# Kernel tuning notes

Measured on AMD Instinct MI355X. Metric: run time of the kernel, lower is better.

## Reference

```python
import jax, jax.numpy as jnp
import numpy as np

G = 32        # group_num
PD = 8        # primary capsule dim
OC = 10       # output caps (classes)
OD = 16       # output dim
GS = 36       # group_size = primary spatial 6*6
N_ITERS = 3   # routing iterations


def conv2d(x, w, stride):
    return jax.lax.conv_general_dilated(
        x, w, window_strides=(stride, stride), padding='VALID',
        dimension_numbers=('NCHW', 'OIHW', 'NCHW'))


def squash(x):
    l2 = jnp.sum(x * x, axis=-1, keepdims=True)
    l = jnp.sqrt(l2)
    return x * (l2 / (1.0 + l2)) / (l + 1e-8)


def setup_inputs() -> dict:
    key = jax.random.key(0)
    ks = jax.random.split(key, 6)
    B = 256
    inp = jax.random.normal(ks[0], (B, 1, 28, 28), dtype=jnp.float32)
    W1 = jax.random.normal(ks[1], (256, 1, 9, 9), dtype=jnp.float32) * 0.05
    b1 = jnp.zeros((256,), dtype=jnp.float32)
    W2 = jax.random.normal(ks[2], (G * PD, 256, 9, 9), dtype=jnp.float32) * 0.01
    b2 = jnp.zeros((G * PD,), dtype=jnp.float32)
    Wcaps = jax.random.normal(ks[3], (G, GS, PD, OC * OD), dtype=jnp.float32) * 0.01
    b_route = jnp.zeros((G, 1, GS, OC), dtype=jnp.float32)
    return {'input': inp, 'W1': W1, 'b1': b1, 'W2': W2, 'b2': b2,
            'Wcaps': Wcaps, 'b_route': b_route}


def reference(input, W1, b1, W2, b2, Wcaps, b_route):
    B = input.shape[0]
    # conv1 + relu: (B,256,20,20)
    x = jax.nn.relu(conv2d(input, W1, 1) + b1[None, :, None, None])
    # primary caps conv: (B,256,6,6)
    y = conv2d(x, W2, 2) + b2[None, :, None, None]
    H = y.shape[2]
    # (B,G,PD,H,W) -> (B,G,H,W,PD) -> (B,G,GS,PD)
    y = y.reshape(B, G, PD, H, H).transpose(0, 1, 3, 4, 2).reshape(B, G, GS, PD)
    u = squash(y)
    # capsule predictions: (B,G,GS,OC,OD)
    up = jnp.einsum('bgsi,gsio->bgso', u, Wcaps).reshape(B, G, GS, OC, OD)
    # routing logits: (B,G,GS,OC)
    b = jnp.broadcast_to(jnp.transpose(b_route, (1, 0, 2, 3)), (B, G, GS, OC))
    v = None
    for r in range(N_ITERS):
        c = jax.nn.softmax(b, axis=3)                       # (B,G,GS,OC)
        s = jnp.einsum('bgso,bgsod->bgod', c, up)           # (B,G,OC,OD)
        v = squash(s)
        if r < N_ITERS - 1:
            b = b + jnp.einsum('bgsod,bgod->bgso', up, v)
    v = v.sum(axis=1)                                       # (B,OC,OD)
    probs = jnp.sqrt(jnp.sum(v * v, axis=2))                # (B,OC)
    return v, probs
```

## Files before the change

kernel.cpp:

```cpp
#include <hip/hip_runtime.h>
#include <math.h>


typedef float floatx4 __attribute__((ext_vector_type(4)));
typedef __bf16 bf16x8 __attribute__((ext_vector_type(8)));
typedef unsigned uintx4 __attribute__((ext_vector_type(4)));

#define XHI_OFF 0u
#define XLO_OFF 52428800u
#define WHI_OFF 104857600u
#define WLO_OFF 116391936u
#define Y2_OFF  127926272u
#define VP_OFF  137363456u
#define Y2_BYTES 9437184u

#define SL_IY   88
#define SL_IMG  1760
#define SL_PAR  7072
#define SL_TOT  14144

#define TAPSTRIDE 65536

__device__ __forceinline__ void bf16split(float v, short& hs, short& ls) {
  unsigned u = __builtin_bit_cast(unsigned, v);
  unsigned r = (u + 0x7FFFu + ((u >> 16) & 1u)) & 0xFFFF0000u;
  hs = (short)(r >> 16);
  float lo = v - __builtin_bit_cast(float, r);
  unsigned u2 = __builtin_bit_cast(unsigned, lo);
  unsigned r2 = u2 + 0x7FFFu + ((u2 >> 16) & 1u);
  ls = (short)(r2 >> 16);
}

__global__ __launch_bounds__(320) void conv1_k(
    const float* __restrict__ inp, const float* __restrict__ W1,
    const float* __restrict__ b1, short* __restrict__ xhi,
    short* __restrict__ xlo) {
  __shared__ __align__(16) float img[784];
  __shared__ float wl[81 * 34];
  const int blk = blockIdx.x;
  const int b = blk >> 3;
  const int cbase = (blk & 7) * 32;
  const int t = threadIdx.x;

  const float4* src = (const float4*)(inp + b * 784);
  for (int idx = t; idx < 196; idx += 320) ((float4*)img)[idx] = src[idx];
  for (int idx = t; idx < 2592; idx += 320) {
    int c = idx / 81, tap = idx - c * 81;
    wl[tap * 34 + c] = W1[(cbase + c) * 81 + tap];
  }
  __syncthreads();

  const int oy = t >> 4;
  const int ct = t & 15;
  const int c0 = cbase + ct * 2;
  const float bias0 = b1[c0], bias1 = b1[c0 + 1];
  float acc0[20], acc1[20];
#pragma unroll
  for (int ox = 0; ox < 20; ox++) { acc0[ox] = bias0; acc1[ox] = bias1; }

#pragma unroll 1
  for (int i = 0; i < 9; i++) {
    float wr0[9], wr1[9];
#pragma unroll
    for (int j = 0; j < 9; j++) {
      float2 wv = *(const float2*)&wl[(i * 9 + j) * 34 + ct * 2];
      wr0[j] = wv.x; wr1[j] = wv.y;
    }
    float xr[28];
    const float4* rp = (const float4*)&img[(oy + i) * 28];
#pragma unroll
    for (int k = 0; k < 7; k++) {
      float4 v = rp[k];
      xr[4 * k] = v.x; xr[4 * k + 1] = v.y; xr[4 * k + 2] = v.z; xr[4 * k + 3] = v.w;
    }
#pragma unroll
    for (int j = 0; j < 9; j++)
#pragma unroll
      for (int ox = 0; ox < 20; ox++) {
        acc0[ox] = fmaf(xr[ox + j], wr0[j], acc0[ox]);
        acc1[ox] = fmaf(xr[ox + j], wr1[j], acc1[ox]);
      }
  }
  const long pbase = (long)(b * 400 + oy * 20) * 256 + c0;
#pragma unroll
  for (int ox = 0; ox < 20; ox++) {
    float v0 = fmaxf(acc0[ox], 0.f), v1 = fmaxf(acc1[ox], 0.f);
    short h0, l0, h1, l1;
    bf16split(v0, h0, l0);
    bf16split(v1, h1, l1);
    long a = pbase + (long)ox * 256;
    *(short2*)&xhi[a] = make_short2(h0, h1);
    *(short2*)&xlo[a] = make_short2(l0, l1);
  }
}

__global__ __launch_bounds__(256) void wtrans_k(
    const float* __restrict__ W2, short* __restrict__ whi,
    short* __restrict__ wlo) {
  __shared__ short lh[81 * 258];
  __shared__ short ll[81 * 258];
  const int blk = blockIdx.x;
  const int icg = blk & 31, ocg = blk >> 5;
  const int t = threadIdx.x;

  for (int idx = t; idx < 20736; idx += 256) {
    int c = idx / 648, r = idx - c * 648;
    int ics = r / 81, tap = r - ics * 81;
    float v = W2[(long)(ocg * 32 + c) * 20736 + icg * 648 + r];
    short h, l;
    bf16split(v, h, l);
    lh[tap * 258 + c * 8 + ics] = h;
    ll[tap * 258 + c * 8 + ics] = l;
  }
  __syncthreads();
  const long obase = (long)icg * 2048 + ocg * 256 + t;
#pragma unroll 1
  for (int tap = 0; tap < 88; tap++) {
    short h = 0, l = 0;
    if (tap < 81) { h = lh[tap * 258 + t]; l = ll[tap * 258 + t]; }
    whi[obase + (long)tap * TAPSTRIDE] = h;
    wlo[obase + (long)tap * TAPSTRIDE] = l;
  }
}

__global__ __launch_bounds__(256, 2) void conv2_k(
    const short* __restrict__ xhi, const short* __restrict__ xlo,
    const short* __restrict__ whi, const short* __restrict__ wlo,
    float* __restrict__ y2) {
  __shared__ __align__(16) short slabA[SL_TOT];

  const int blk = blockIdx.x;
  const int ks = blk & 7;
  const int mb = blk >> 3;
  const int b0 = mb * 4;
  const int t = threadIdx.x;
  const int lane = t & 63;
  const int q = lane >> 4;
  const int ln16 = lane & 15;
  const int wv = t >> 6;

  int combo[9];
#pragma unroll
  for (int mt = 0; mt < 9; mt++) {
    int row = mt * 16 + ln16;
    int im = row / 36;
    int pos = row - im * 36;
    int oy = pos / 6, ox = pos - oy * 6;
    combo[mt] = im * SL_IMG + oy * (2 * SL_IY) + ox * 8;
  }

  floatx4 acc[9][4];
#pragma unroll
  for (int mt = 0; mt < 9; mt++)
#pragma unroll
    for (int nt = 0; nt < 4; nt++) acc[mt][nt] = (floatx4)0.f;

#pragma unroll 1
  for (int icg = 0; icg < 4; icg++) {
    const int icgG = ks * 4 + icg;
    const long icoff = (long)icgG * 8;
    const long wb0 = ((long)icgG * 256 + wv * 64 + ln16) * 8 + (long)q * TAPSTRIDE;

    __syncthreads();
    for (int idx = t; idx < 1600; idx += 256) {
      int im = idx / 400, p = idx - im * 400;
      int iy = p / 20, ix = p - iy * 20;
      int dst = (ix & 1) * SL_PAR + im * SL_IMG + iy * SL_IY + (ix >> 1) * 8;
      const long src = ((long)(b0 + im) * 400 + p) * 256 + icoff;
      uintx4 vh = __builtin_nontemporal_load((const uintx4*)&xhi[src]);
      *(uintx4*)&slabA[dst] = vh;
    }
    __syncthreads();

    {
      bf16x8 cbh[4];
#pragma unroll
      for (int nt = 0; nt < 4; nt++) cbh[nt] = *(const bf16x8*)&whi[wb0 + nt * 128];
#pragma unroll 1
      for (int kst = 0; kst < 21; kst++) {
        const int t0n = (kst < 20) ? (kst + 1) * 4 : 80;
        bf16x8 nbh[4], cbl[4];
#pragma unroll
        for (int nt = 0; nt < 4; nt++) {
          nbh[nt] = *(const bf16x8*)&whi[wb0 + (long)t0n * TAPSTRIDE + nt * 128];
          cbl[nt] = *(const bf16x8*)&wlo[wb0 + (long)(kst * 4) * TAPSTRIDE + nt * 128];
        }
        const int tap = kst * 4 + q;
        const int i = tap / 9, j = tap - i * 9;
        const int aoff = (j & 1) * SL_PAR + i * SL_IY + (j >> 1) * 8;
#pragma unroll
        for (int bb = 0; bb < 3; bb++) {
          bf16x8 av[3];
#pragma unroll
          for (int m3 = 0; m3 < 3; m3++)
            av[m3] = *(const bf16x8*)&slabA[aoff + combo[bb * 3 + m3]];
#pragma unroll
          for (int nt = 0; nt < 4; nt++)
#pragma unroll
            for (int m3 = 0; m3 < 3; m3++)
              acc[bb * 3 + m3][nt] = __builtin_amdgcn_mfma_f32_16x16x32_bf16(
                  av[m3], cbh[nt], acc[bb * 3 + m3][nt], 0, 0, 0);
#pragma unroll
          for (int nt = 0; nt < 4; nt++)
#pragma unroll
            for (int m3 = 0; m3 < 3; m3++)
              acc[bb * 3 + m3][nt] = __builtin_amdgcn_mfma_f32_16x16x32_bf16(
                  av[m3], cbl[nt], acc[bb * 3 + m3][nt], 0, 0, 0);
        }
#pragma unroll
        for (int nt = 0; nt < 4; nt++) cbh[nt] = nbh[nt];
      }
    }

    __syncthreads();
    for (int idx = t; idx < 1600; idx += 256) {
      int im = idx / 400, p = idx - im * 400;
      int iy = p / 20, ix = p - iy * 20;
      int dst = (ix & 1) * SL_PAR + im * SL_IMG + iy * SL_IY + (ix >> 1) * 8;
      const long src = ((long)(b0 + im) * 400 + p) * 256 + icoff;
      uintx4 vl = __builtin_nontemporal_load((const uintx4*)&xlo[src]);
      *(uintx4*)&slabA[dst] = vl;
    }
    __syncthreads();

    {
      bf16x8 cbh[4];
#pragma unroll
      for (int nt = 0; nt < 4; nt++) cbh[nt] = *(const bf16x8*)&whi[wb0 + nt * 128];
#pragma unroll 1
      for (int kst = 0; kst < 21; kst++) {
        const int t0n = (kst < 20) ? (kst + 1) * 4 : 80;
        bf16x8 nbh[4];
#pragma unroll
        for (int nt = 0; nt < 4; nt++)
          nbh[nt] = *(const bf16x8*)&whi[wb0 + (long)t0n * TAPSTRIDE + nt * 128];
        const int tap = kst * 4 + q;
        const int i = tap / 9, j = tap - i * 9;
        const int aoff = (j & 1) * SL_PAR + i * SL_IY + (j >> 1) * 8;
#pragma unroll
        for (int bb = 0; bb < 3; bb++) {
          bf16x8 av[3];
#pragma unroll
          for (int m3 = 0; m3 < 3; m3++)
            av[m3] = *(const bf16x8*)&slabA[aoff + combo[bb * 3 + m3]];
#pragma unroll
          for (int nt = 0; nt < 4; nt++)
#pragma unroll
            for (int m3 = 0; m3 < 3; m3++)
              acc[bb * 3 + m3][nt] = __builtin_amdgcn_mfma_f32_16x16x32_bf16(
                  av[m3], cbh[nt], acc[bb * 3 + m3][nt], 0, 0, 0);
        }
#pragma unroll
        for (int nt = 0; nt < 4; nt++) cbh[nt] = nbh[nt];
      }
    }
  }

#pragma unroll
  for (int mt = 0; mt < 9; mt++)
#pragma unroll
    for (int nt = 0; nt < 4; nt++) {
      int oc = wv * 64 + nt * 16 + ln16;
      int rowb = mb * 144 + mt * 16 + q * 4;
#pragma unroll
      for (int r = 0; r < 4; r++)
        atomicAdd(&y2[(long)(rowb + r) * 256 + oc], acc[mt][nt][r]);
    }
}

__global__ __launch_bounds__(256) void caps_k(
    const float* __restrict__ y2, const float* __restrict__ b2,
    const float* __restrict__ Wcaps, const float* __restrict__ b_route,
    float* __restrict__ vpart) {
  __shared__ float u[288];
  __shared__ float usc[36];
  __shared__ float up[5760];
  __shared__ float bl[360];
  __shared__ float cl[360];
  __shared__ float sv[160];
  __shared__ float vv[160];
  __shared__ float scale[10];
  const int blk = blockIdx.x;
  const int g = blk & 31, b = blk >> 5;
  const int t = threadIdx.x;

  for (int idx = t; idx < 288; idx += 256) {
    int s = idx >> 3, d = idx & 7;
    u[idx] = y2[((long)b * 36 + s) * 256 + g * 8 + d] + b2[g * 8 + d];
  }
  for (int idx = t; idx < 360; idx += 256) bl[idx] = b_route[g * 360 + idx];
  __syncthreads();
  if (t < 36) {
    float l2 = 0.f;
#pragma unroll
    for (int d = 0; d < 8; d++) { float v = u[t * 8 + d]; l2 = fmaf(v, v, l2); }
    float l = sqrtf(l2);
    usc[t] = (l2 / (1.f + l2)) / (l + 1e-8f);
  }
  __syncthreads();
  for (int idx = t; idx < 288; idx += 256) u[idx] *= usc[idx >> 3];
  __syncthreads();
  for (int idx = t; idx < 5760; idx += 256) {
    int s = idx / 160, k = idx - s * 160;
    const float* wp = Wcaps + (g * 36 + s) * 8 * 160 + k;
    float a = 0.f;
#pragma unroll
    for (int d = 0; d < 8; d++) a = fmaf(u[s * 8 + d], wp[d * 160], a);
    up[idx] = a;
  }
  __syncthreads();

  for (int r = 0; r < 3; r++) {
    if (t < 36) {
      float m = bl[t * 10];
#pragma unroll
      for (int oc = 1; oc < 10; oc++) m = fmaxf(m, bl[t * 10 + oc]);
      float e[10]; float sum = 0.f;
#pragma unroll
      for (int oc = 0; oc < 10; oc++) { e[oc] = expf(bl[t * 10 + oc] - m); sum += e[oc]; }
      float inv = 1.f / sum;
#pragma unroll
      for (int oc = 0; oc < 10; oc++) cl[t * 10 + oc] = e[oc] * inv;
    }
    __syncthreads();
    if (t < 160) {
      const int oc = t >> 4;
      float a = 0.f;
#pragma unroll 1
      for (int s = 0; s < 36; s++) a = fmaf(cl[s * 10 + oc], up[s * 160 + t], a);
      sv[t] = a;
    }
    __syncthreads();
    if (t < 10) {
      float l2 = 0.f;
#pragma unroll
      for (int od = 0; od < 16; od++) { float v = sv[t * 16 + od]; l2 = fmaf(v, v, l2); }
      scale[t] = (l2 / (1.f + l2)) / (sqrtf(l2) + 1e-8f);
    }
    __syncthreads();
    if (t < 160) vv[t] = sv[t] * scale[t >> 4];
    __syncthreads();
    if (r < 2) {
      for (int idx = t; idx < 360; idx += 256) {
        int s = idx / 10, oc = idx - s * 10;
        float a = 0.f;
#pragma unroll
        for (int od = 0; od < 16; od++)
          a = fmaf(up[s * 160 + oc * 16 + od], vv[oc * 16 + od], a);
        bl[idx] += a;
      }
      __syncthreads();
    }
  }
  if (t < 160) vpart[(b * 32 + g) * 160 + t] = vv[t];
}

__global__ __launch_bounds__(192) void final_k(
    const float* __restrict__ vpart, float* __restrict__ out) {
  __shared__ float v[160];
  const int b = blockIdx.x, t = threadIdx.x;
  if (t < 160) {
    float a = 0.f;
#pragma unroll 4
    for (int g = 0; g < 32; g++) a += vpart[(b * 32 + g) * 160 + t];
    v[t] = a;
    out[b * 160 + t] = a;
  }
  __syncthreads();
  if (t < 10) {
    float l2 = 0.f;
#pragma unroll
    for (int od = 0; od < 16; od++) { float x = v[t * 16 + od]; l2 = fmaf(x, x, l2); }
    out[40960 + b * 10 + t] = sqrtf(l2);
  }
}

extern "C" void kernel_launch(void* const* d_in, const int* in_sizes, int n_in,
                              void* d_out, int out_size, void* d_ws, size_t ws_size,
                              hipStream_t stream) {
  const float* inp     = (const float*)d_in[0];
  const float* W1      = (const float*)d_in[1];
  const float* b1      = (const float*)d_in[2];
  const float* W2      = (const float*)d_in[3];
  const float* b2      = (const float*)d_in[4];
  const float* Wcaps   = (const float*)d_in[5];
  const float* b_route = (const float*)d_in[6];
  float* out = (float*)d_out;
  char* ws = (char*)d_ws;

  short* xhi = (short*)(ws + XHI_OFF);
  short* xlo = (short*)(ws + XLO_OFF);
  short* whi = (short*)(ws + WHI_OFF);
  short* wlo = (short*)(ws + WLO_OFF);
  float* y2  = (float*)(ws + Y2_OFF);
  float* vp  = (float*)(ws + VP_OFF);

  (void)hipMemsetAsync(y2, 0, Y2_BYTES, stream);
  conv1_k <<<2048, 320, 0, stream>>>(inp, W1, b1, xhi, xlo);
  wtrans_k<<<256, 256, 0, stream>>>(W2, whi, wlo);
  conv2_k <<<512, 256, 0, stream>>>(xhi, xlo, whi, wlo, y2);
  caps_k  <<<8192, 256, 0, stream>>>(y2, b2, Wcaps, b_route, vp);
  final_k <<<256, 192, 0, stream>>>(vp, out);
}
```

Baseline: 549.5 us.

## Write conv1 output in slab layout and double-buffer conv2 staging via LDS DMA

conv1 now stores its hi/lo bf16 activations directly in the padded, parity-split slab layout that conv2 uses. The padding columns are zero-filled, and the workspace offsets are reshuffled to fit. conv2 then copies each slab straight into LDS with global_load_lds and two buffers, so the next hi/lo slab loads while the current one feeds the MFMAs. This removes the per-element index math, the register round trip and one barrier per stage. In exchange it relies on the barrier's implicit wait for the async LDS loads to finish, and the workspace layout gets a little larger.

```diff
diff --git a/kernel.cpp b/kernel.cpp
--- a/kernel.cpp
+++ b/kernel.cpp
@@ -7,17 +7,17 @@
 typedef unsigned uintx4 __attribute__((ext_vector_type(4)));
 
 #define XHI_OFF 0u
-#define XLO_OFF 52428800u
-#define WHI_OFF 104857600u
-#define WLO_OFF 116391936u
-#define Y2_OFF  127926272u
-#define VP_OFF  137363456u
+#define XLO_OFF 58720256u
+#define WHI_OFF 117440512u
+#define WLO_OFF 128974848u
+#define Y2_OFF  140509184u
+#define VP_OFF  0u
 #define Y2_BYTES 9437184u
 
 #define SL_IY   88
 #define SL_IMG  1760
 #define SL_PAR  7072
-#define SL_TOT  14144
+#define SL_STRIDE 14336
 
 #define TAPSTRIDE 65536
 
@@ -29,6 +29,14 @@
   unsigned u2 = __builtin_bit_cast(unsigned, lo);
   unsigned r2 = u2 + 0x7FFFu + ((u2 >> 16) & 1u);
   ls = (short)(r2 >> 16);
+}
+
+__device__ __forceinline__ void stage7(const short* gp, short* lp) {
+#pragma unroll
+  for (int c = 0; c < 7; c++)
+    __builtin_amdgcn_global_load_lds(
+        (const __attribute__((address_space(1))) void*)(gp + c * 512),
+        (__attribute__((address_space(3))) void*)(lp + c * 512), 16, 0, 0);
 }
 
 __global__ __launch_bounds__(320) void conv1_k(
@@ -81,16 +89,27 @@
         acc1[ox] = fmaf(xr[ox + j], wr1[j], acc1[ox]);
       }
   }
-  const long pbase = (long)(b * 400 + oy * 20) * 256 + c0;
+
+  const int icgG = c0 >> 3;
+  const long sbase = ((long)(icgG * 64 + (b >> 2))) * SL_STRIDE
+                   + (long)(b & 3) * SL_IMG + (long)oy * SL_IY + (c0 & 7);
 #pragma unroll
   for (int ox = 0; ox < 20; ox++) {
     float v0 = fmaxf(acc0[ox], 0.f), v1 = fmaxf(acc1[ox], 0.f);
     short h0, l0, h1, l1;
     bf16split(v0, h0, l0);
     bf16split(v1, h1, l1);
-    long a = pbase + (long)ox * 256;
+    long a = sbase + (ox & 1) * SL_PAR + (ox >> 1) * 8;
     *(short2*)&xhi[a] = make_short2(h0, h1);
     *(short2*)&xlo[a] = make_short2(l0, l1);
+  }
+  {
+    long a0 = sbase + 80;
+    *(short2*)&xhi[a0] = make_short2(0, 0);
+    *(short2*)&xlo[a0] = make_short2(0, 0);
+    long a1 = sbase + SL_PAR + 80;
+    *(short2*)&xhi[a1] = make_short2(0, 0);
+    *(short2*)&xlo[a1] = make_short2(0, 0);
   }
 }
 
@@ -127,12 +146,11 @@
     const short* __restrict__ xhi, const short* __restrict__ xlo,
     const short* __restrict__ whi, const short* __restrict__ wlo,
     float* __restrict__ y2) {
-  __shared__ __align__(16) short slabA[SL_TOT];
+  __shared__ __align__(16) short slab[2][SL_STRIDE];
 
   const int blk = blockIdx.x;
   const int ks = blk & 7;
   const int mb = blk >> 3;
-  const int b0 = mb * 4;
   const int t = threadIdx.x;
   const int lane = t & 63;
   const int q = lane >> 4;
@@ -155,22 +173,17 @@
 #pragma unroll
     for (int nt = 0; nt < 4; nt++) acc[mt][nt] = (floatx4)0.f;
 
+  const int stoff = wv * 7 * 512 + lane * 8;
+
+  stage7(xhi + (long)(ks * 4 * 64 + mb) * SL_STRIDE + stoff, &slab[0][stoff]);
+
 #pragma unroll 1
   for (int icg = 0; icg < 4; icg++) {
     const int icgG = ks * 4 + icg;
-    const long icoff = (long)icgG * 8;
     const long wb0 = ((long)icgG * 256 + wv * 64 + ln16) * 8 + (long)q * TAPSTRIDE;
 
     __syncthreads();
-    for (int idx = t; idx < 1600; idx += 256) {
-      int im = idx / 400, p = idx - im * 400;
-      int iy = p / 20, ix = p - iy * 20;
-      int dst = (ix & 1) * SL_PAR + im * SL_IMG + iy * SL_IY + (ix >> 1) * 8;
-      const long src = ((long)(b0 + im) * 400 + p) * 256 + icoff;
-      uintx4 vh = __builtin_nontemporal_load((const uintx4*)&xhi[src]);
-      *(uintx4*)&slabA[dst] = vh;
-    }
-    __syncthreads();
+    stage7(xlo + (long)(icgG * 64 + mb) * SL_STRIDE + stoff, &slab[1][stoff]);
 
     {
       bf16x8 cbh[4];
@@ -193,7 +206,7 @@
           bf16x8 av[3];
 #pragma unroll
           for (int m3 = 0; m3 < 3; m3++)
-            av[m3] = *(const bf16x8*)&slabA[aoff + combo[bb * 3 + m3]];
+            av[m3] = *(const bf16x8*)&slab[0][aoff + combo[bb * 3 + m3]];
 #pragma unroll
           for (int nt = 0; nt < 4; nt++)
 #pragma unroll
@@ -213,15 +226,8 @@
     }
 
     __syncthreads();
-    for (int idx = t; idx < 1600; idx += 256) {
-      int im = idx / 400, p = idx - im * 400;
-      int iy = p / 20, ix = p - iy * 20;
-      int dst = (ix & 1) * SL_PAR + im * SL_IMG + iy * SL_IY + (ix >> 1) * 8;
-      const long src = ((long)(b0 + im) * 400 + p) * 256 + icoff;
-      uintx4 vl = __builtin_nontemporal_load((const uintx4*)&xlo[src]);
-      *(uintx4*)&slabA[dst] = vl;
-    }
-    __syncthreads();
+    if (icg < 3)
+      stage7(xhi + (long)((icgG + 1) * 64 + mb) * SL_STRIDE + stoff, &slab[0][stoff]);
 
     {
       bf16x8 cbh[4];
@@ -242,7 +248,7 @@
           bf16x8 av[3];
 #pragma unroll
           for (int m3 = 0; m3 < 3; m3++)
-            av[m3] = *(const bf16x8*)&slabA[aoff + combo[bb * 3 + m3]];
+            av[m3] = *(const bf16x8*)&slab[1][aoff + combo[bb * 3 + m3]];
 #pragma unroll
           for (int nt = 0; nt < 4; nt++)
 #pragma unroll
```

Measured after the change: 520.9 us. -5.2%, faster.
